# Kernel optimization log

Hardware: AMD Instinct MI355X
Metric: run time of the kernel (lower is better)

The kernel has to match this reference:

```python
import jax, jax.numpy as jnp
import numpy as np

DT = 0.001  # forward's default dt
EPS = 1e-10


def setup_inputs() -> dict:
    key = jax.random.key(0)
    k1, k2 = jax.random.split(key)
    nt, ntr, nc = 4096, 1024, 3
    x = jax.random.normal(k1, (nt, ntr, nc), dtype=jnp.float32)
    y = jax.random.normal(k2, (nt, ntr, nc), dtype=jnp.float32)
    return {"x": x, "y": y}


def reference(x, y):
    # x, y: [nt, ntraces, nchannels]
    nt = x.shape[0]
    # autocorrelation energy per (trace, channel) column via Parseval-style FFT sum
    X = jnp.fft.fft(x, axis=0)
    Y = jnp.fft.fft(y, axis=0)
    Ex = DT * jnp.sum(jnp.abs(X) ** 2, axis=0) / nt + EPS  # [ntr, nc]
    Ey = DT * jnp.sum(jnp.abs(Y) ** 2, axis=0) / nt + EPS  # [ntr, nc]
    dots = jnp.sum(x * y, axis=0)                          # [ntr, nc]
    cc = dots / jnp.sqrt(Ex * Ey)                          # [ntr, nc]
    # original skips columns whose max |x| is exactly 0
    mask = jnp.max(jnp.abs(x), axis=0) > 0
    loss = jnp.sum(jnp.where(mask, cc, 0.0))
    return loss
```

## Files before the change

### kernel.cpp

```cpp
#include <hip/hip_runtime.h>


#define NT 4096
#define NCOL 3072
#define NCOL4 768
#define CHUNKS 256
#define TSTEPS (NT / CHUNKS)

#define PS_F4_PER_STAT (CHUNKS * NCOL4)
#define BSUM_OFFSET_BYTES (3 * PS_F4_PER_STAT * 16)

__global__ __launch_bounds__(256) void ncc_stage1(const float* __restrict__ x,
                                                  const float* __restrict__ y,
                                                  float4* __restrict__ ps) {
    const int bx   = blockIdx.x;
    const int g    = bx % 3;
    const int ch   = bx / 3;
    const int tid  = threadIdx.x;
    const int col4 = g * 256 + tid;

    const float4* __restrict__ x4 = reinterpret_cast<const float4*>(x);
    const float4* __restrict__ y4 = reinterpret_cast<const float4*>(y);

    float4 sx2 = {0.f, 0.f, 0.f, 0.f};
    float4 sy2 = {0.f, 0.f, 0.f, 0.f};
    float4 sxy = {0.f, 0.f, 0.f, 0.f};

    const int t0 = ch * TSTEPS;
#pragma unroll
    for (int tt = 0; tt < TSTEPS; ++tt) {
        const int idx = (t0 + tt) * NCOL4 + col4;
        float4 xv = x4[idx];
        float4 yv = y4[idx];
        sx2.x = fmaf(xv.x, xv.x, sx2.x);
        sx2.y = fmaf(xv.y, xv.y, sx2.y);
        sx2.z = fmaf(xv.z, xv.z, sx2.z);
        sx2.w = fmaf(xv.w, xv.w, sx2.w);
        sy2.x = fmaf(yv.x, yv.x, sy2.x);
        sy2.y = fmaf(yv.y, yv.y, sy2.y);
        sy2.z = fmaf(yv.z, yv.z, sy2.z);
        sy2.w = fmaf(yv.w, yv.w, sy2.w);
        sxy.x = fmaf(xv.x, yv.x, sxy.x);
        sxy.y = fmaf(xv.y, yv.y, sxy.y);
        sxy.z = fmaf(xv.z, yv.z, sxy.z);
        sxy.w = fmaf(xv.w, yv.w, sxy.w);
    }

    const int slot = ch * NCOL4 + col4;
    ps[0 * PS_F4_PER_STAT + slot] = sx2;
    ps[1 * PS_F4_PER_STAT + slot] = sy2;
    ps[2 * PS_F4_PER_STAT + slot] = sxy;
}

__global__ __launch_bounds__(256) void ncc_stage2(const float* __restrict__ ps,
                                                  float* __restrict__ bsum) {
    const int b    = blockIdx.x;
    const int tid  = threadIdx.x;
    const int lane = tid & 63;
    const int q    = tid >> 6;
    const int j    = b * 64 + lane;

    float sx2 = 0.f, sy2 = 0.f, sxy = 0.f;
    const int c0 = q * (CHUNKS / 4);
#pragma unroll 4
    for (int c = c0; c < c0 + CHUNKS / 4; ++c) {
        sx2 += ps[0 * CHUNKS * NCOL + c * NCOL + j];
        sy2 += ps[1 * CHUNKS * NCOL + c * NCOL + j];
        sxy += ps[2 * CHUNKS * NCOL + c * NCOL + j];
    }

    __shared__ float red[3][4][64];
    red[0][q][lane] = sx2;
    red[1][q][lane] = sy2;
    red[2][q][lane] = sxy;
    __syncthreads();

    if (q == 0) {
        sx2 = red[0][0][lane] + red[0][1][lane] + red[0][2][lane] + red[0][3][lane];
        sy2 = red[1][0][lane] + red[1][1][lane] + red[1][2][lane] + red[1][3][lane];
        sxy = red[2][0][lane] + red[2][1][lane] + red[2][2][lane] + red[2][3][lane];
        float ex = fmaf(0.001f, sx2, 1e-10f);
        float ey = fmaf(0.001f, sy2, 1e-10f);
        float cc = (sx2 > 0.f) ? sxy * rsqrtf(ex * ey) : 0.f;
#pragma unroll
        for (int off = 32; off > 0; off >>= 1)
            cc += __shfl_down(cc, off, 64);
        if (lane == 0) bsum[b] = cc;
    }
}

__global__ __launch_bounds__(64) void ncc_stage3(const float* __restrict__ bsum,
                                                 float* __restrict__ out) {
    const int lane = threadIdx.x;
    float v = (lane < 48) ? bsum[lane] : 0.f;
#pragma unroll
    for (int off = 32; off > 0; off >>= 1)
        v += __shfl_down(v, off, 64);
    if (lane == 0) out[0] = v;
}

extern "C" void kernel_launch(void* const* d_in, const int* in_sizes, int n_in,
                              void* d_out, int out_size, void* d_ws, size_t ws_size,
                              hipStream_t stream) {
    const float* x = reinterpret_cast<const float*>(d_in[0]);
    const float* y = reinterpret_cast<const float*>(d_in[1]);
    float* out = reinterpret_cast<float*>(d_out);
    float4* ps = reinterpret_cast<float4*>(d_ws);
    float* bsum = reinterpret_cast<float*>(reinterpret_cast<char*>(d_ws) + BSUM_OFFSET_BYTES);

    ncc_stage1<<<dim3(3 * CHUNKS), dim3(256), 0, stream>>>(x, y, ps);
    ncc_stage2<<<dim3(48), dim3(256), 0, stream>>>(reinterpret_cast<const float*>(ps), bsum);
    ncc_stage3<<<dim3(1), dim3(64), 0, stream>>>(bsum, out);
}
```

Before: 126.6 us.

## Fuse final reduction into stage2 via atomic counter and use nontemporal loads

```diff
diff --git a/kernel.cpp b/kernel.cpp
--- a/kernel.cpp
+++ b/kernel.cpp
@@ -7,53 +7,52 @@
 #define CHUNKS 256
 #define TSTEPS (NT / CHUNKS)
 
+typedef float vfloat4 __attribute__((ext_vector_type(4)));
+
 #define PS_F4_PER_STAT (CHUNKS * NCOL4)
-#define BSUM_OFFSET_BYTES (3 * PS_F4_PER_STAT * 16)
+#define ACC_OFFSET_F   (3 * PS_F4_PER_STAT * 4)
 
 __global__ __launch_bounds__(256) void ncc_stage1(const float* __restrict__ x,
                                                   const float* __restrict__ y,
-                                                  float4* __restrict__ ps) {
+                                                  float* __restrict__ ws) {
     const int bx   = blockIdx.x;
     const int g    = bx % 3;
     const int ch   = bx / 3;
     const int tid  = threadIdx.x;
     const int col4 = g * 256 + tid;
 
-    const float4* __restrict__ x4 = reinterpret_cast<const float4*>(x);
-    const float4* __restrict__ y4 = reinterpret_cast<const float4*>(y);
+    if (bx == 0 && tid == 0) {
+        ws[ACC_OFFSET_F] = 0.f;
+        reinterpret_cast<unsigned int*>(ws)[ACC_OFFSET_F + 1] = 0u;
+    }
 
-    float4 sx2 = {0.f, 0.f, 0.f, 0.f};
-    float4 sy2 = {0.f, 0.f, 0.f, 0.f};
-    float4 sxy = {0.f, 0.f, 0.f, 0.f};
+    const vfloat4* __restrict__ x4 = reinterpret_cast<const vfloat4*>(x);
+    const vfloat4* __restrict__ y4 = reinterpret_cast<const vfloat4*>(y);
+    vfloat4* __restrict__ ps = reinterpret_cast<vfloat4*>(ws);
+
+    vfloat4 sx2 = {0.f, 0.f, 0.f, 0.f};
+    vfloat4 sy2 = {0.f, 0.f, 0.f, 0.f};
+    vfloat4 sxy = {0.f, 0.f, 0.f, 0.f};
 
     const int t0 = ch * TSTEPS;
 #pragma unroll
     for (int tt = 0; tt < TSTEPS; ++tt) {
         const int idx = (t0 + tt) * NCOL4 + col4;
-        float4 xv = x4[idx];
-        float4 yv = y4[idx];
-        sx2.x = fmaf(xv.x, xv.x, sx2.x);
-        sx2.y = fmaf(xv.y, xv.y, sx2.y);
-        sx2.z = fmaf(xv.z, xv.z, sx2.z);
-        sx2.w = fmaf(xv.w, xv.w, sx2.w);
-        sy2.x = fmaf(yv.x, yv.x, sy2.x);
-        sy2.y = fmaf(yv.y, yv.y, sy2.y);
-        sy2.z = fmaf(yv.z, yv.z, sy2.z);
-        sy2.w = fmaf(yv.w, yv.w, sy2.w);
-        sxy.x = fmaf(xv.x, yv.x, sxy.x);
-        sxy.y = fmaf(xv.y, yv.y, sxy.y);
-        sxy.z = fmaf(xv.z, yv.z, sxy.z);
-        sxy.w = fmaf(xv.w, yv.w, sxy.w);
+        vfloat4 xv = __builtin_nontemporal_load(x4 + idx);
+        vfloat4 yv = __builtin_nontemporal_load(y4 + idx);
+        sx2 = xv * xv + sx2;
+        sy2 = yv * yv + sy2;
+        sxy = xv * yv + sxy;
     }
 
     const int slot = ch * NCOL4 + col4;
-    ps[0 * PS_F4_PER_STAT + slot] = sx2;
-    ps[1 * PS_F4_PER_STAT + slot] = sy2;
-    ps[2 * PS_F4_PER_STAT + slot] = sxy;
+    __builtin_nontemporal_store(sx2, ps + 0 * PS_F4_PER_STAT + slot);
+    __builtin_nontemporal_store(sy2, ps + 1 * PS_F4_PER_STAT + slot);
+    __builtin_nontemporal_store(sxy, ps + 2 * PS_F4_PER_STAT + slot);
 }
 
-__global__ __launch_bounds__(256) void ncc_stage2(const float* __restrict__ ps,
-                                                  float* __restrict__ bsum) {
+__global__ __launch_bounds__(256) void ncc_stage2(const float* __restrict__ ws,
+                                                  float* __restrict__ out) {
     const int b    = blockIdx.x;
     const int tid  = threadIdx.x;
     const int lane = tid & 63;
@@ -62,11 +61,11 @@
 
     float sx2 = 0.f, sy2 = 0.f, sxy = 0.f;
     const int c0 = q * (CHUNKS / 4);
-#pragma unroll 4
+#pragma unroll 8
     for (int c = c0; c < c0 + CHUNKS / 4; ++c) {
-        sx2 += ps[0 * CHUNKS * NCOL + c * NCOL + j];
-        sy2 += ps[1 * CHUNKS * NCOL + c * NCOL + j];
-        sxy += ps[2 * CHUNKS * NCOL + c * NCOL + j];
+        sx2 += ws[0 * CHUNKS * NCOL + c * NCOL + j];
+        sy2 += ws[1 * CHUNKS * NCOL + c * NCOL + j];
+        sxy += ws[2 * CHUNKS * NCOL + c * NCOL + j];
     }
 
     __shared__ float red[3][4][64];
@@ -85,18 +84,20 @@
 #pragma unroll
         for (int off = 32; off > 0; off >>= 1)
             cc += __shfl_down(cc, off, 64);
-        if (lane == 0) bsum[b] = cc;
+        if (lane == 0) {
+            float* acc = const_cast<float*>(ws) + ACC_OFFSET_F;
+            unsigned int* counter =
+                reinterpret_cast<unsigned int*>(const_cast<float*>(ws)) + ACC_OFFSET_F + 1;
+            atomicAdd(acc, cc);
+            __threadfence();
+            unsigned int old = atomicAdd(counter, 1u);
+            if (old == 47u) {
+                __threadfence();
+                float total = atomicAdd(acc, 0.f);
+                out[0] = total;
+            }
+        }
     }
-}
-
-__global__ __launch_bounds__(64) void ncc_stage3(const float* __restrict__ bsum,
-                                                 float* __restrict__ out) {
-    const int lane = threadIdx.x;
-    float v = (lane < 48) ? bsum[lane] : 0.f;
-#pragma unroll
-    for (int off = 32; off > 0; off >>= 1)
-        v += __shfl_down(v, off, 64);
-    if (lane == 0) out[0] = v;
 }
 
 extern "C" void kernel_launch(void* const* d_in, const int* in_sizes, int n_in,
@@ -105,10 +106,8 @@
     const float* x = reinterpret_cast<const float*>(d_in[0]);
     const float* y = reinterpret_cast<const float*>(d_in[1]);
     float* out = reinterpret_cast<float*>(d_out);
-    float4* ps = reinterpret_cast<float4*>(d_ws);
-    float* bsum = reinterpret_cast<float*>(reinterpret_cast<char*>(d_ws) + BSUM_OFFSET_BYTES);
+    float* ws = reinterpret_cast<float*>(d_ws);
 
-    ncc_stage1<<<dim3(3 * CHUNKS), dim3(256), 0, stream>>>(x, y, ps);
-    ncc_stage2<<<dim3(48), dim3(256), 0, stream>>>(reinterpret_cast<const float*>(ps), bsum);
-    ncc_stage3<<<dim3(1), dim3(64), 0, stream>>>(bsum, out);
+    ncc_stage1<<<dim3(3 * CHUNKS), dim3(256), 0, stream>>>(x, y, ws);
+    ncc_stage2<<<dim3(48), dim3(256), 0, stream>>>(ws, out);
 }
```

New measurement: 127.3 us. About the same (+0.6%).
